# Optimization experiments

Measured on AMD Instinct MI355X. Metric: run time of the kernel, lower is better.

The kernel has to match this reference:

```python
import jax, jax.numpy as jnp
import numpy as np

DIM = 1024
HEADS = 8
DIM_HEAD = 64
INNER = HEADS * DIM_HEAD  # 512
LN_EPS = 1e-5


def setup_inputs() -> dict:
    key = jax.random.key(0)
    ks = jax.random.split(key, 8)
    b, n, m = 4, 2048, 512
    x = jax.random.normal(ks[0], (b, n, DIM), dtype=jnp.float32)
    media = jax.random.normal(ks[1], (b, m, DIM), dtype=jnp.float32)
    media_mask = jax.random.randint(ks[2], (b, m), 0, 2).astype(jnp.bool_)
    media_mask = media_mask.at[:, 0].set(True)  # avoid fully-masked rows
    ln_g = jnp.ones((DIM,), jnp.float32)
    ln_b = jnp.zeros((DIM,), jnp.float32)
    s = 0.02
    Wq = jax.random.normal(ks[3], (DIM, INNER), jnp.float32) * s
    Wkv = jax.random.normal(ks[4], (DIM, 2 * INNER), jnp.float32) * s
    Wo = jax.random.normal(ks[5], (INNER, DIM), jnp.float32) * s
    return {"x": x, "media": media, "media_mask": media_mask,
            "ln_g": ln_g, "ln_b": ln_b, "Wq": Wq, "Wkv": Wkv, "Wo": Wo}


def _layernorm(x, g, b):
    mu = jnp.mean(x, axis=-1, keepdims=True)
    var = jnp.var(x, axis=-1, keepdims=True)
    return (x - mu) * jax.lax.rsqrt(var + LN_EPS) * g + b


def reference(x, media, media_mask, ln_g, ln_b, Wq, Wkv, Wo):
    scale = DIM_HEAD ** (-0.5)
    xn = _layernorm(x, ln_g, ln_b)
    q = xn @ Wq                                  # (b, n, inner)
    kv = media @ Wkv                             # (b, m, 2*inner)
    k, v = jnp.split(kv, 2, axis=-1)
    # b n (h d) -> b h n d
    def split_heads(t):
        b_, s_, _ = t.shape
        return t.reshape(b_, s_, HEADS, DIM_HEAD).transpose(0, 2, 1, 3)
    q, k, v = split_heads(q) * scale, split_heads(k), split_heads(v)
    sim = jnp.einsum('bhid,bhjd->bhij', q, k)    # (b, h, n, m)
    neg_inf = jnp.finfo(sim.dtype).min
    sim = jnp.where(media_mask[:, None, None, :], sim, neg_inf)
    attn = jax.nn.softmax(sim, axis=-1)          # stable (max-subtract) softmax
    out = jnp.einsum('bhij,bhjd->bhid', attn, v)  # (b, h, n, d)
    out = out.transpose(0, 2, 1, 3).reshape(x.shape[0], x.shape[1], INNER)
    return out @ Wo
```

## Files before the change

kernel.cpp:

```cpp
#include <hip/hip_runtime.h>
#include <hip/hip_bf16.h>

typedef unsigned short u16;
typedef __attribute__((ext_vector_type(4))) unsigned short u16x4;
typedef __attribute__((ext_vector_type(8))) unsigned short u16x8;
typedef __attribute__((ext_vector_type(8))) short bf16x8;
typedef __attribute__((ext_vector_type(4))) float f32x4;

#define AS1 __attribute__((address_space(1)))
#define AS3 __attribute__((address_space(3)))

__device__ __forceinline__ float b2f(u16 v) {
    return __uint_as_float(((unsigned)v) << 16);
}
__device__ __forceinline__ u16 f2bf(float f) {
    unsigned u = __float_as_uint(f);
    unsigned r = (u + 0x7fffu + ((u >> 16) & 1u)) >> 16;
    return (u16)r;
}

__global__ __launch_bounds__(256) void prep_all(
    const float* __restrict__ x, const float* __restrict__ media,
    const unsigned char* __restrict__ mask,
    const float* __restrict__ ln_g, const float* __restrict__ ln_b,
    const float* __restrict__ Wq, const float* __restrict__ Wkv,
    const float* __restrict__ Wo,
    u16* __restrict__ xn, u16* __restrict__ mediab,
    unsigned char* __restrict__ mask8, int* __restrict__ idx,
    int* __restrict__ cnts,
    u16* __restrict__ wqt, u16* __restrict__ wkvt, u16* __restrict__ wot) {
    __shared__ u16 T[64][72];
    __shared__ int c0s, c1s;
    const int bid = blockIdx.x, tid = threadIdx.x;

    if (bid < 2048) {
        const int lane = tid & 63;
        const int row = bid * 4 + (tid >> 6);
        const float* xr = x + (size_t)row * 1024;
        float v[16];
        float sum = 0.f, sq = 0.f;
#pragma unroll
        for (int c = 0; c < 4; ++c) {
            float4 u = ((const float4*)xr)[c * 64 + lane];
            v[c * 4 + 0] = u.x; v[c * 4 + 1] = u.y; v[c * 4 + 2] = u.z; v[c * 4 + 3] = u.w;
            sum += u.x + u.y + u.z + u.w;
            sq += u.x * u.x + u.y * u.y + u.z * u.z + u.w * u.w;
        }
#pragma unroll
        for (int o = 1; o < 64; o <<= 1) {
            sum += __shfl_xor(sum, o, 64);
            sq += __shfl_xor(sq, o, 64);
        }
        float mean = sum * (1.f / 1024.f);
        float var = sq * (1.f / 1024.f) - mean * mean;
        float rs = rsqrtf(var + 1e-5f);
        u16* yr = xn + (size_t)row * 1024;
#pragma unroll
        for (int c = 0; c < 4; ++c) {
            float4 ug = ((const float4*)ln_g)[c * 64 + lane];
            float4 ub = ((const float4*)ln_b)[c * 64 + lane];
            u16x4 o;
            o[0] = f2bf((v[c * 4 + 0] - mean) * rs * ug.x + ub.x);
            o[1] = f2bf((v[c * 4 + 1] - mean) * rs * ug.y + ub.y);
            o[2] = f2bf((v[c * 4 + 2] - mean) * rs * ug.z + ub.z);
            o[3] = f2bf((v[c * 4 + 3] - mean) * rs * ug.w + ub.w);
            *(u16x4*)(yr + c * 256 + lane * 4) = o;
        }
    } else if (bid < 3072) {
        int i = (bid - 2048) * 256 + tid;
        float4 a = ((const float4*)media)[i * 2];
        float4 b = ((const float4*)media)[i * 2 + 1];
        u16x8 o;
        o[0] = f2bf(a.x); o[1] = f2bf(a.y); o[2] = f2bf(a.z); o[3] = f2bf(a.w);
        o[4] = f2bf(b.x); o[5] = f2bf(b.y); o[6] = f2bf(b.z); o[7] = f2bf(b.w);
        ((u16x8*)mediab)[i] = o;
    } else if (bid < 3840) {
        const int t = bid - 3072;
        const int z = t >> 8, rem = t & 255;
        const float* in; u16* out; int K, N;
        if (z == 0)      { in = Wq;  out = wqt;  K = 1024; N = 512; }
        else if (z == 1) { in = Wkv; out = wkvt; K = 1024; N = 1024; }
        else             { in = Wo;  out = wot;  K = 512;  N = 1024; }
        const int k0 = (rem >> 4) * 64, n0 = (rem & 15) * 64;
        if (k0 >= K || n0 >= N) return;
#pragma unroll
        for (int p = 0; p < 4; ++p) {
            int kr = p * 16 + (tid >> 4);
            float4 u = *(const float4*)(in + (size_t)(k0 + kr) * N + n0 + (tid & 15) * 4);
            u16x4 o4;
            o4[0] = f2bf(u.x); o4[1] = f2bf(u.y); o4[2] = f2bf(u.z); o4[3] = f2bf(u.w);
            *(u16x4*)(&T[kr][(tid & 15) * 4]) = o4;
        }
        __syncthreads();
        const int n = tid >> 2, kc = (tid & 3) * 16;
#pragma unroll
        for (int hh = 0; hh < 2; ++hh) {
            u16x8 o;
#pragma unroll
            for (int i = 0; i < 8; ++i) o[i] = T[kc + hh * 8 + i][n];
            *(u16x8*)(out + (size_t)(n0 + n) * K + k0 + kc + hh * 8) = o;
        }
    } else {
        if (tid == 0) { c0s = 0; c1s = 0; }
        __syncthreads();
        int a0 = 0, a1 = 0;
        for (int i = tid; i < 2048; i += 256) {
            if (mask[i]) {
                int cl = i & 3;
                if (cl == 0) a0 = 1;
                else if (cl == 1) a1 = 1;
            }
        }
        if (a0) atomicOr(&c0s, 1);
        if (a1) atomicOr(&c1s, 1);
        __syncthreads();
        int fmt = c1s ? 1 : (c0s ? 0 : 2);
        for (int e = tid; e < 2048; e += 256) {
            unsigned char v;
            if (fmt == 1)      v = (mask[e] != 0);
            else if (fmt == 0) v = (((const int*)mask)[e] != 0);
            else               v = (((const float*)mask)[e] != 0.f);
            mask8[e] = v;
        }
        __syncthreads();
        const int wv = tid >> 6, l = tid & 63;
        int off = 0;
#pragma unroll
        for (int c = 0; c < 8; ++c) {
            int key = c * 64 + l;
            bool v = mask8[wv * 512 + key] != 0;
            unsigned long long m = __ballot(v);
            int rank = __popcll(m & ((1ull << l) - 1ull));
            if (v) idx[wv * 512 + off + rank] = key;
            off += __popcll(m);
        }
        if (l == 0) cnts[wv] = off;
        int nt = (off + 63) & ~63;
        for (int p = off + l; p < nt; p += 64) idx[wv * 512 + p] = 0;
    }
}

template <int OUTF32>
__device__ __forceinline__ void gemm_tile_g(u16* As, u16* Bs,
                                            const u16* __restrict__ A,
                                            const u16* __restrict__ Bt,
                                            void* __restrict__ Cv,
                                            int N, int K, int row0, int col0,
                                            float scale) {
    const int tid = threadIdx.x;
    const int l = tid & 63, w = tid >> 6;
    const int l15 = l & 15, l4 = l >> 4;
    const int wm = w >> 1, wn = w & 1;
    const int lr = l >> 3;
    const int cs = ((l & 7) ^ lr) * 8;

    f32x4 zero = {0.f, 0.f, 0.f, 0.f};
    f32x4 acc[4][4];
#pragma unroll
    for (int i = 0; i < 4; ++i)
#pragma unroll
        for (int j = 0; j < 4; ++j) acc[i][j] = zero;

    const int rsw = l15 & 7;

    for (int k0 = 0; k0 < K; k0 += 64) {
        __syncthreads();
#pragma unroll
        for (int i = 0; i < 4; ++i) {
            int r = w * 32 + i * 8;
            __builtin_amdgcn_global_load_lds(
                (const AS1 void*)(A + (size_t)(row0 + r + lr) * K + k0 + cs),
                (AS3 void*)(As + r * 64), 16, 0, 0);
            __builtin_amdgcn_global_load_lds(
                (const AS1 void*)(Bt + (size_t)(col0 + r + lr) * K + k0 + cs),
                (AS3 void*)(Bs + r * 64), 16, 0, 0);
        }
        __syncthreads();
#pragma unroll
        for (int h = 0; h < 2; ++h) {
            bf16x8 aF[4], bF[4];
#pragma unroll
            for (int m = 0; m < 4; ++m) {
                int s = (h * 4 + l4) ^ rsw;
                aF[m] = *(const bf16x8*)(As + (wm * 64 + m * 16 + l15) * 64 + s * 8);
                bF[m] = *(const bf16x8*)(Bs + (wn * 64 + m * 16 + l15) * 64 + s * 8);
            }
#pragma unroll
            for (int m = 0; m < 4; ++m)
#pragma unroll
                for (int n = 0; n < 4; ++n)
                    acc[m][n] = __builtin_amdgcn_mfma_f32_16x16x32_bf16(aF[m], bF[n], acc[m][n], 0, 0, 0);
        }
    }
#pragma unroll
    for (int m = 0; m < 4; ++m)
#pragma unroll
        for (int n = 0; n < 4; ++n) {
            int row = row0 + wm * 64 + m * 16 + l4 * 4;
            int col = col0 + wn * 64 + n * 16 + l15;
#pragma unroll
            for (int r = 0; r < 4; ++r) {
                float vv = acc[m][n][r] * scale;
                if (OUTF32)
                    ((float*)Cv)[(size_t)(row + r) * N + col] = vv;
                else
                    ((u16*)Cv)[(size_t)(row + r) * N + col] = f2bf(vv);
            }
        }
}

__global__ __launch_bounds__(256, 2) void qkv_gemm(const u16* __restrict__ xn,
                                                   const u16* __restrict__ wqt,
                                                   u16* __restrict__ qb,
                                                   const u16* __restrict__ mediab,
                                                   const u16* __restrict__ wkvt,
                                                   u16* __restrict__ kvb) {
    __shared__ u16 As[128 * 64];
    __shared__ u16 Bs[128 * 64];
    const int b = blockIdx.x;
    const u16 *A, *Bt; u16* C; int N, row0, col0; float sc;
    if (b < 256) { A = xn;     Bt = wqt;  C = qb;  N = 512;  row0 = (b >> 2) * 128; col0 = (b & 3) * 128; sc = 0.125f; }
    else { int t = b - 256; A = mediab; Bt = wkvt; C = kvb; N = 1024; row0 = (t >> 3) * 128; col0 = (t & 7) * 128; sc = 1.f; }
    gemm_tile_g<0>(As, Bs, A, Bt, (void*)C, N, 1024, row0, col0, sc);
}

__global__ __launch_bounds__(256, 2) void o_gemm(const u16* __restrict__ ao,
                                                 const u16* __restrict__ wot,
                                                 float* __restrict__ out) {
    __shared__ u16 As[128 * 64];
    __shared__ u16 Bs[128 * 64];
    gemm_tile_g<1>(As, Bs, ao, wot, (void*)out, 1024, 512,
                   (int)blockIdx.y * 128, (int)blockIdx.x * 128, 1.f);
}

__global__ __launch_bounds__(256) void attn_mfma(const u16* __restrict__ qb,
                                                 const u16* __restrict__ kvb,
                                                 const int* __restrict__ idx,
                                                 const int* __restrict__ cnts,
                                                 u16* __restrict__ ao) {
    __shared__ u16 Ks[64][72];
    __shared__ u16 Vt[64][72];
    __shared__ u16 Pl[4][16][72];
    __shared__ int Is[512];
    const int tid = threadIdx.x;
    const int l = tid & 63, w = tid >> 6;
    const int l15 = l & 15, l4 = l >> 4;
    const int h = blockIdx.y, bbi = blockIdx.z;
    const int n0 = blockIdx.x * 64;
    const int cnt = cnts[bbi];
    const int ntile = (cnt + 63) & ~63;
    const int* ib = idx + bbi * 512;
    for (int i = tid; i < ntile; i += 256) Is[i] = ib[i];

    const u16* qp = qb + ((size_t)(bbi * 2048 + n0 + w * 16 + l15)) * 512 + h * 64;
    const bf16x8 qf0 = *(const bf16x8*)(qp + l4 * 8);
    const bf16x8 qf1 = *(const bf16x8*)(qp + 32 + l4 * 8);

    const f32x4 zero = {0.f, 0.f, 0.f, 0.f};
    f32x4 acc[4];
#pragma unroll
    for (int dt = 0; dt < 4; ++dt) acc[dt] = zero;
    float mrun[4] = {-3.0e38f, -3.0e38f, -3.0e38f, -3.0e38f};
    float lrun[4] = {0.f, 0.f, 0.f, 0.f};

    const int kj = tid >> 3, kd = (tid & 7) * 8;
    const int vj = tid & 63, vd = (tid >> 6) * 16;
    const u16* kbase = kvb + ((size_t)bbi * 512) * 1024 + h * 64;

    for (int j0 = 0; j0 < cnt; j0 += 64) {
        __syncthreads();
#pragma unroll
        for (int p = 0; p < 2; ++p) {
            int r = kj + p * 32;
            int row = Is[j0 + r];
            u16x8 kv_ = *(const u16x8*)(kbase + (size_t)row * 1024 + kd);
            *(u16x8*)(&Ks[r][kd]) = kv_;
        }
        {
            int row = Is[j0 + vj];
#pragma unroll
            for (int p = 0; p < 2; ++p) {
                u16x8 vv = *(const u16x8*)(kbase + (size_t)row * 1024 + 512 + vd + p * 8);
#pragma unroll
                for (int i = 0; i < 8; ++i) Vt[vd + p * 8 + i][vj] = vv[i];
            }
        }
        __syncthreads();

        f32x4 s[4];
        float mv[4];
#pragma unroll
        for (int jt = 0; jt < 4; ++jt) {
            bf16x8 kf0 = *(const bf16x8*)(&Ks[jt * 16 + l15][l4 * 8]);
            bf16x8 kf1 = *(const bf16x8*)(&Ks[jt * 16 + l15][32 + l4 * 8]);
            s[jt] = __builtin_amdgcn_mfma_f32_16x16x32_bf16(qf0, kf0, zero, 0, 0, 0);
            s[jt] = __builtin_amdgcn_mfma_f32_16x16x32_bf16(qf1, kf1, s[jt], 0, 0, 0);
            mv[jt] = (j0 + jt * 16 + l15 < cnt) ? 0.f : -3.0e38f;
        }

        float sv[4][4];
        float pmax[4];
        bool cond = true;
#pragma unroll
        for (int r = 0; r < 4; ++r) {
#pragma unroll
            for (int jt = 0; jt < 4; ++jt) sv[r][jt] = s[jt][r] + mv[jt];
            pmax[r] = fmaxf(fmaxf(sv[r][0], sv[r][1]), fmaxf(sv[r][2], sv[r][3]));
            cond = cond && (pmax[r] <= mrun[r] + 8.f);
        }
        if (__all(cond)) {
#pragma unroll
            for (int r = 0; r < 4; ++r) {
                float p0 = __expf(sv[r][0] - mrun[r]);
                float p1 = __expf(sv[r][1] - mrun[r]);
                float p2 = __expf(sv[r][2] - mrun[r]);
                float p3 = __expf(sv[r][3] - mrun[r]);
                lrun[r] += (p0 + p1) + (p2 + p3);
                Pl[w][l4 * 4 + r][l15] = f2bf(p0);
                Pl[w][l4 * 4 + r][16 + l15] = f2bf(p1);
                Pl[w][l4 * 4 + r][32 + l15] = f2bf(p2);
                Pl[w][l4 * 4 + r][48 + l15] = f2bf(p3);
            }
        } else {
#pragma unroll
            for (int r = 0; r < 4; ++r) {
                float tmax = pmax[r];
#pragma unroll
                for (int o = 1; o < 16; o <<= 1) tmax = fmaxf(tmax, __shfl_xor(tmax, o, 64));
                float mn = fmaxf(mrun[r], tmax);
                float corr = __expf(mrun[r] - mn);
                mrun[r] = mn;
                float p0 = __expf(sv[r][0] - mn);
                float p1 = __expf(sv[r][1] - mn);
                float p2 = __expf(sv[r][2] - mn);
                float p3 = __expf(sv[r][3] - mn);
                lrun[r] = lrun[r] * corr + (p0 + p1) + (p2 + p3);
#pragma unroll
                for (int dt = 0; dt < 4; ++dt) acc[dt][r] *= corr;
                Pl[w][l4 * 4 + r][l15] = f2bf(p0);
                Pl[w][l4 * 4 + r][16 + l15] = f2bf(p1);
                Pl[w][l4 * 4 + r][32 + l15] = f2bf(p2);
                Pl[w][l4 * 4 + r][48 + l15] = f2bf(p3);
            }
        }
        bf16x8 pf0 = *(const bf16x8*)(&Pl[w][l15][l4 * 8]);
        bf16x8 pf1 = *(const bf16x8*)(&Pl[w][l15][32 + l4 * 8]);
#pragma unroll
        for (int dt = 0; dt < 4; ++dt) {
            bf16x8 vf0 = *(const bf16x8*)(&Vt[dt * 16 + l15][l4 * 8]);
            bf16x8 vf1 = *(const bf16x8*)(&Vt[dt * 16 + l15][32 + l4 * 8]);
            acc[dt] = __builtin_amdgcn_mfma_f32_16x16x32_bf16(pf0, vf0, acc[dt], 0, 0, 0);
            acc[dt] = __builtin_amdgcn_mfma_f32_16x16x32_bf16(pf1, vf1, acc[dt], 0, 0, 0);
        }
    }

    float inv[4];
#pragma unroll
    for (int r = 0; r < 4; ++r) {
        float lt = lrun[r];
#pragma unroll
        for (int o = 1; o < 16; o <<= 1) lt += __shfl_xor(lt, o, 64);
        inv[r] = (lt > 0.f) ? (1.f / lt) : 0.f;
    }
    u16* op = ao + ((size_t)(bbi * 2048 + n0 + w * 16)) * 512 + h * 64;
#pragma unroll
    for (int dt = 0; dt < 4; ++dt)
#pragma unroll
        for (int r = 0; r < 4; ++r)
            op[(size_t)(l4 * 4 + r) * 512 + dt * 16 + l15] = f2bf(acc[dt][r] * inv[r]);
}

extern "C" void kernel_launch(void* const* d_in, const int* in_sizes, int n_in,
                              void* d_out, int out_size, void* d_ws, size_t ws_size,
                              hipStream_t stream) {
    const float* x = (const float*)d_in[0];
    const float* media = (const float*)d_in[1];
    const unsigned char* mask = (const unsigned char*)d_in[2];
    const float* ln_g = (const float*)d_in[3];
    const float* ln_b = (const float*)d_in[4];
    const float* Wq = (const float*)d_in[5];
    const float* Wkv = (const float*)d_in[6];
    const float* Wo = (const float*)d_in[7];
    float* out = (float*)d_out;

    char* w = (char*)d_ws;
    unsigned char* mask8 = (unsigned char*)w; w += 4096;
    int* idx = (int*)w;    w += 2048 * 4;
    int* cnts = (int*)w;   w += 256;
    u16* qb = (u16*)w;     w += (size_t)8192 * 512 * 2;
    u16* kvb = (u16*)w;    w += (size_t)2048 * 1024 * 2;
    u16* ao = (u16*)w;     w += (size_t)8192 * 512 * 2;
    u16* mediab = (u16*)w; w += (size_t)2048 * 1024 * 2;
    u16* wqt = (u16*)w;    w += (size_t)512 * 1024 * 2;
    u16* wkvt = (u16*)w;   w += (size_t)1024 * 1024 * 2;
    u16* wot = (u16*)w;    w += (size_t)1024 * 512 * 2;
    u16* xn = (u16*)d_out;

    prep_all<<<3841, 256, 0, stream>>>(x, media, mask, ln_g, ln_b, Wq, Wkv, Wo,
                                       xn, mediab, mask8, idx, cnts, wqt, wkvt, wot);
    qkv_gemm<<<384, 256, 0, stream>>>(xn, wqt, qb, mediab, wkvt, kvb);
    attn_mfma<<<dim3(32, 8, 4), 256, 0, stream>>>(qb, kvb, idx, cnts, ao);
    o_gemm<<<dim3(8, 64), 256, 0, stream>>>(ao, wot, out);
}
```

Baseline: 77.83 us.

## Gather unmasked media rows into KV GEMM and skip masked tiles

The KV projection GEMM now gathers only the unmasked media rows, using the compacted index list as the A-row source, so K/V are stored contiguously and densely per batch. Row tiles beyond the padded valid count exit early, which skips roughly half the KV GEMM work for masked keys. The attention kernel then reads K/V rows directly without the shared-memory index table. Index padding grows to multiples of 128 to match the GEMM tile. The cost is an indirect per-row address in the GEMM loads.

```diff
diff --git a/kernel.cpp b/kernel.cpp
--- a/kernel.cpp
+++ b/kernel.cpp
@@ -135,18 +135,19 @@
             off += __popcll(m);
         }
         if (l == 0) cnts[wv] = off;
-        int nt = (off + 63) & ~63;
+        int nt = (off + 127) & ~127;
         for (int p = off + l; p < nt; p += 64) idx[wv * 512 + p] = 0;
     }
 }
 
-template <int OUTF32>
+template <int OUTF32, int GATHER>
 __device__ __forceinline__ void gemm_tile_g(u16* As, u16* Bs,
                                             const u16* __restrict__ A,
                                             const u16* __restrict__ Bt,
                                             void* __restrict__ Cv,
                                             int N, int K, int row0, int col0,
-                                            float scale) {
+                                            float scale,
+                                            const int* __restrict__ ridx) {
     const int tid = threadIdx.x;
     const int l = tid & 63, w = tid >> 6;
     const int l15 = l & 15, l4 = l >> 4;
@@ -154,6 +155,13 @@
     const int lr = l >> 3;
     const int cs = ((l & 7) ^ lr) * 8;
 
+    int arow[4];
+#pragma unroll
+    for (int i = 0; i < 4; ++i) {
+        int g = w * 32 + i * 8 + lr;
+        arow[i] = GATHER ? ridx[row0 + g] : (row0 + g);
+    }
+
     f32x4 zero = {0.f, 0.f, 0.f, 0.f};
     f32x4 acc[4][4];
 #pragma unroll
@@ -169,7 +177,7 @@
         for (int i = 0; i < 4; ++i) {
             int r = w * 32 + i * 8;
             __builtin_amdgcn_global_load_lds(
-                (const AS1 void*)(A + (size_t)(row0 + r + lr) * K + k0 + cs),
+                (const AS1 void*)(A + (size_t)arow[i] * K + k0 + cs),
                 (AS3 void*)(As + r * 64), 16, 0, 0);
             __builtin_amdgcn_global_load_lds(
                 (const AS1 void*)(Bt + (size_t)(col0 + r + lr) * K + k0 + cs),
@@ -214,14 +222,25 @@
                                                    u16* __restrict__ qb,
                                                    const u16* __restrict__ mediab,
                                                    const u16* __restrict__ wkvt,
-                                                   u16* __restrict__ kvb) {
+                                                   u16* __restrict__ kvb,
+                                                   const int* __restrict__ idx,
+                                                   const int* __restrict__ cnts) {
     __shared__ u16 As[128 * 64];
     __shared__ u16 Bs[128 * 64];
     const int b = blockIdx.x;
-    const u16 *A, *Bt; u16* C; int N, row0, col0; float sc;
-    if (b < 256) { A = xn;     Bt = wqt;  C = qb;  N = 512;  row0 = (b >> 2) * 128; col0 = (b & 3) * 128; sc = 0.125f; }
-    else { int t = b - 256; A = mediab; Bt = wkvt; C = kvb; N = 1024; row0 = (t >> 3) * 128; col0 = (t & 7) * 128; sc = 1.f; }
-    gemm_tile_g<0>(As, Bs, A, Bt, (void*)C, N, 1024, row0, col0, sc);
+    if (b < 256) {
+        gemm_tile_g<0, 0>(As, Bs, xn, wqt, (void*)qb, 512, 1024,
+                          (b >> 2) * 128, (b & 3) * 128, 0.125f, nullptr);
+    } else {
+        const int t = b - 256;
+        const int bbi = t >> 5, rem = t & 31;
+        const int row0 = (rem >> 3) * 128, col0 = (rem & 7) * 128;
+        const int nt128 = (cnts[bbi] + 127) & ~127;
+        if (row0 >= nt128) return;
+        gemm_tile_g<0, 1>(As, Bs, mediab + (size_t)bbi * 512 * 1024, wkvt,
+                          (void*)(kvb + (size_t)bbi * 512 * 1024), 1024, 1024,
+                          row0, col0, 1.f, idx + bbi * 512);
+    }
 }
 
 __global__ __launch_bounds__(256, 2) void o_gemm(const u16* __restrict__ ao,
@@ -229,28 +248,23 @@
                                                  float* __restrict__ out) {
     __shared__ u16 As[128 * 64];
     __shared__ u16 Bs[128 * 64];
-    gemm_tile_g<1>(As, Bs, ao, wot, (void*)out, 1024, 512,
-                   (int)blockIdx.y * 128, (int)blockIdx.x * 128, 1.f);
+    gemm_tile_g<1, 0>(As, Bs, ao, wot, (void*)out, 1024, 512,
+                      (int)blockIdx.y * 128, (int)blockIdx.x * 128, 1.f, nullptr);
 }
 
 __global__ __launch_bounds__(256) void attn_mfma(const u16* __restrict__ qb,
                                                  const u16* __restrict__ kvb,
-                                                 const int* __restrict__ idx,
                                                  const int* __restrict__ cnts,
                                                  u16* __restrict__ ao) {
     __shared__ u16 Ks[64][72];
     __shared__ u16 Vt[64][72];
     __shared__ u16 Pl[4][16][72];
-    __shared__ int Is[512];
     const int tid = threadIdx.x;
     const int l = tid & 63, w = tid >> 6;
     const int l15 = l & 15, l4 = l >> 4;
     const int h = blockIdx.y, bbi = blockIdx.z;
     const int n0 = blockIdx.x * 64;
     const int cnt = cnts[bbi];
-    const int ntile = (cnt + 63) & ~63;
-    const int* ib = idx + bbi * 512;
-    for (int i = tid; i < ntile; i += 256) Is[i] = ib[i];
 
     const u16* qp = qb + ((size_t)(bbi * 2048 + n0 + w * 16 + l15)) * 512 + h * 64;
     const bf16x8 qf0 = *(const bf16x8*)(qp + l4 * 8);
@@ -272,15 +286,13 @@
 #pragma unroll
         for (int p = 0; p < 2; ++p) {
             int r = kj + p * 32;
-            int row = Is[j0 + r];
-            u16x8 kv_ = *(const u16x8*)(kbase + (size_t)row * 1024 + kd);
+            u16x8 kv_ = *(const u16x8*)(kbase + (size_t)(j0 + r) * 1024 + kd);
             *(u16x8*)(&Ks[r][kd]) = kv_;
         }
         {
-            int row = Is[j0 + vj];
 #pragma unroll
             for (int p = 0; p < 2; ++p) {
-                u16x8 vv = *(const u16x8*)(kbase + (size_t)row * 1024 + 512 + vd + p * 8);
+                u16x8 vv = *(const u16x8*)(kbase + (size_t)(j0 + vj) * 1024 + 512 + vd + p * 8);
 #pragma unroll
                 for (int i = 0; i < 8; ++i) Vt[vd + p * 8 + i][vj] = vv[i];
             }
@@ -398,7 +410,7 @@
 
     prep_all<<<3841, 256, 0, stream>>>(x, media, mask, ln_g, ln_b, Wq, Wkv, Wo,
                                        xn, mediab, mask8, idx, cnts, wqt, wkvt, wot);
-    qkv_gemm<<<384, 256, 0, stream>>>(xn, wqt, qb, mediab, wkvt, kvb);
-    attn_mfma<<<dim3(32, 8, 4), 256, 0, stream>>>(qb, kvb, idx, cnts, ao);
+    qkv_gemm<<<384, 256, 0, stream>>>(xn, wqt, qb, mediab, wkvt, kvb, idx, cnts);
+    attn_mfma<<<dim3(32, 8, 4), 256, 0, stream>>>(qb, kvb, cnts, ao);
     o_gemm<<<dim3(8, 64), 256, 0, stream>>>(ao, wot, out);
 }
```

Result: no change. 76.57 us, median of 2 (-1.6%).
